# Kernel optimization log

Hardware: AMD Instinct MI355X
Metric: run time of the kernel (lower is better)

The kernel has to match this reference:

```python
import jax, jax.numpy as jnp
import numpy as np

B, F, V_IN = 8, 64, 163842  # icosahedron order 7
V_OUT, K = 40962, 7         # order 6, 1-ring (6 neighbors + self)


def setup_inputs() -> dict:
    key = jax.random.key(0)
    kx, ki = jax.random.split(key)
    x = jax.random.normal(kx, (B, F, V_IN), dtype=jnp.float32)
    neigh_indices = jax.random.randint(ki, (V_OUT, K), 0, V_IN, dtype=jnp.int64)
    return {"x": x, "neigh_indices": neigh_indices}


def reference(x, neigh_indices):
    # Gather fixed-size 1-ring neighborhoods: (B, F, V_OUT, K)
    gathered = x[:, :, neigh_indices]
    # Mean pooling over the neighborhood axis (pooling_type='mean')
    pooled = jnp.mean(gathered, axis=-1)  # (B, F, V_OUT)
    # Original returns (pooled, max_pool_indices=None); indices are None for mean.
    return pooled
```

## Files before the change

### kernel.cpp

```cpp
#include <hip/hip_runtime.h>


typedef float    f4 __attribute__((ext_vector_type(4)));
typedef float    f8 __attribute__((ext_vector_type(8)));
typedef _Float16 h8 __attribute__((ext_vector_type(8)));
typedef unsigned int u4 __attribute__((ext_vector_type(4)));

constexpr int B = 8, F = 64, V_IN = 163842, V_OUT = 40962, K = 7;
constexpr int ROWS = B * F;
constexpr int RG   = 32;
constexpr int NG   = ROWS / RG;
constexpr int TPB  = 256;
constexpr int GPX  = NG / 8;
constexpr int CPB  = 128;
constexpr int IBX  = (V_IN + CPB - 1) / CPB;
constexpr int LSH  = 34;
constexpr int VPB  = 64;
constexpr int VB   = (V_OUT + VPB - 1) / VPB;
constexpr int BLOCKS2 = 8 * GPX * VB;
constexpr size_t XH_BYTES = (size_t)NG * V_IN * 64;

__global__ __launch_bounds__(TPB) void icopool_pack_h(
    const float* __restrict__ x, u4* __restrict__ xH)
{
    __shared__ _Float16 tile[CPB * LSH];
    const int g  = blockIdx.y;
    const int c0 = blockIdx.x * CPB;
    const int t  = threadIdx.x;
    const int r  = t >> 3;
    const int ci = t & 7;

    const float* xr = x + (size_t)(g * RG + r) * V_IN;
    if (c0 + CPB <= V_IN) {
        #pragma unroll
        for (int it = 0; it < 4; ++it) {
            const int c4 = ci * 4 + it * 32;
            const f4 vv = *(const f4*)(xr + c0 + c4);
            tile[(c4 + 0) * LSH + r] = (_Float16)vv.x;
            tile[(c4 + 1) * LSH + r] = (_Float16)vv.y;
            tile[(c4 + 2) * LSH + r] = (_Float16)vv.z;
            tile[(c4 + 3) * LSH + r] = (_Float16)vv.w;
        }
    } else {
        for (int it = 0; it < 4; ++it) {
            const int c4 = ci * 4 + it * 32;
            for (int jj = 0; jj < 4; ++jj) {
                const int c = c0 + c4 + jj;
                tile[(c4 + jj) * LSH + r] =
                    (c < V_IN) ? (_Float16)xr[c] : (_Float16)0.0f;
            }
        }
    }
    __syncthreads();

    const unsigned int* ld = (const unsigned int*)tile;
    u4* dst = xH + ((size_t)g * V_IN + c0) * 4;
    #pragma unroll
    for (int it = 0; it < 2; ++it) {
        const int c   = (t >> 2) + it * 64;
        const int sub = t & 3;
        if (c0 + c < V_IN) {
            u4 w;
            w.x = ld[c * 17 + sub * 4 + 0];
            w.y = ld[c * 17 + sub * 4 + 1];
            w.z = ld[c * 17 + sub * 4 + 2];
            w.w = ld[c * 17 + sub * 4 + 3];
            __builtin_nontemporal_store(w, dst + (size_t)c * 4 + sub);
        }
    }
}

__global__ __launch_bounds__(TPB) void icopool_gather_h(
    const h8* __restrict__ xH,
    const int* __restrict__ nidx,
    float*     __restrict__ out)
{
    const int b   = blockIdx.x;
    const int xcd = b & 7;
    const int j   = b >> 3;
    const int gl  = j / VB;
    const int vb  = j % VB;
    const int sub = threadIdx.x & 3;
    const int lv  = threadIdx.x >> 2;
    const int v   = vb * VPB + lv;
    if (v >= V_OUT) return;
    const int g   = xcd * GPX + gl;

    const int base = v * K;
    const int i0 = nidx[base + 0];
    const int i1 = nidx[base + 1];
    const int i2 = nidx[base + 2];
    const int i3 = nidx[base + 3];
    const int i4 = nidx[base + 4];
    const int i5 = nidx[base + 5];
    const int i6 = nidx[base + 6];

    const h8* s = xH + ((size_t)g * V_IN) * 4 + sub;
    f8 acc = __builtin_convertvector(s[(size_t)i0 * 4], f8);
    acc += __builtin_convertvector(s[(size_t)i1 * 4], f8);
    acc += __builtin_convertvector(s[(size_t)i2 * 4], f8);
    acc += __builtin_convertvector(s[(size_t)i3 * 4], f8);
    acc += __builtin_convertvector(s[(size_t)i4 * 4], f8);
    acc += __builtin_convertvector(s[(size_t)i5 * 4], f8);
    acc += __builtin_convertvector(s[(size_t)i6 * 4], f8);
    acc *= (1.0f / 7.0f);

    float* o = out + (size_t)(g * RG + sub * 8) * V_OUT + v;
    #pragma unroll
    for (int rr = 0; rr < 8; ++rr)
        __builtin_nontemporal_store(acc[rr], o + (size_t)rr * V_OUT);
}

constexpr int RPB  = 2;
constexpr int RGS  = ROWS / RPB;
constexpr int RG_PER_XCD = RGS / 8;
constexpr int VB1  = (V_OUT + TPB - 1) / TPB;
constexpr int BLOCKS_V1  = RGS * VB1;

__global__ __launch_bounds__(TPB) void icopool_gather(
    const float* __restrict__ x,
    const int*   __restrict__ nidx,
    float*       __restrict__ out)
{
    const int b        = blockIdx.x;
    const int xcd      = b & 7;
    const int j        = b >> 3;
    const int rg_local = j / VB1;
    const int vb       = j % VB1;
    const int rg       = xcd * RG_PER_XCD + rg_local;
    const int r0       = rg * RPB;

    const int v = vb * TPB + threadIdx.x;
    if (v >= V_OUT) return;

    const int base = v * K;
    const int i0 = nidx[base + 0];
    const int i1 = nidx[base + 1];
    const int i2 = nidx[base + 2];
    const int i3 = nidx[base + 3];
    const int i4 = nidx[base + 4];
    const int i5 = nidx[base + 5];
    const int i6 = nidx[base + 6];

    #pragma unroll
    for (int r = 0; r < RPB; ++r) {
        const float* xr = x + (size_t)(r0 + r) * V_IN;
        float sum = xr[i0] + xr[i1] + xr[i2] + xr[i3] + xr[i4] + xr[i5] + xr[i6];
        __builtin_nontemporal_store(sum * (1.0f / 7.0f),
                                    out + (size_t)(r0 + r) * V_OUT + v);
    }
}

extern "C" void kernel_launch(void* const* d_in, const int* in_sizes, int n_in,
                              void* d_out, int out_size, void* d_ws, size_t ws_size,
                              hipStream_t stream) {
    const float* x    = (const float*)d_in[0];
    const int*   nidx = (const int*)d_in[1];
    float*       out  = (float*)d_out;

    if (ws_size >= XH_BYTES && d_ws != nullptr) {
        u4* xH = (u4*)d_ws;
        icopool_pack_h<<<dim3(IBX, NG), dim3(TPB), 0, stream>>>(x, xH);
        icopool_gather_h<<<dim3(BLOCKS2), dim3(TPB), 0, stream>>>((const h8*)xH, nidx, out);
    } else {
        icopool_gather<<<dim3(BLOCKS_V1), dim3(TPB), 0, stream>>>(x, nidx, out);
    }
}
```

Before: 578.8 us.

## Repack fp16 input into 16-row groups and gather two groups per thread

The pack kernel now transposes x into fp16 records of 16 rows (32 bytes per vertex) instead of 32 rows (64 bytes), using 256-column tiles and nontemporal loads. The gather kernel assigns each wave 64 consecutive output vertices and has each thread read half of a record from two adjacent groups. The goal is fully coalesced output stores and more loads in flight per thread. The cost is that each random gather access shrinks to 16 bytes, and each record to 32 bytes, which may waste memory-transaction granularity on scattered reads.

```diff
diff --git a/kernel.cpp b/kernel.cpp
--- a/kernel.cpp
+++ b/kernel.cpp
@@ -8,34 +8,34 @@
 
 constexpr int B = 8, F = 64, V_IN = 163842, V_OUT = 40962, K = 7;
 constexpr int ROWS = B * F;
-constexpr int RG   = 32;
+constexpr int RG   = 16;
 constexpr int NG   = ROWS / RG;
 constexpr int TPB  = 256;
 constexpr int GPX  = NG / 8;
-constexpr int CPB  = 128;
+constexpr int CPB  = 256;
 constexpr int IBX  = (V_IN + CPB - 1) / CPB;
-constexpr int LSH  = 34;
-constexpr int VPB  = 64;
+constexpr int LSH  = 18;
+constexpr int VPB  = 128;
 constexpr int VB   = (V_OUT + VPB - 1) / VPB;
-constexpr int BLOCKS2 = 8 * GPX * VB;
-constexpr size_t XH_BYTES = (size_t)NG * V_IN * 64;
-
-__global__ __launch_bounds__(TPB) void icopool_pack_h(
+constexpr int NGL  = 2;
+constexpr int BLOCKS2 = 8 * NGL * VB;
+constexpr size_t XH_BYTES = (size_t)NG * V_IN * 32;
+
+__global__ __launch_bounds__(TPB) void icopool_pack_h16(
     const float* __restrict__ x, u4* __restrict__ xH)
 {
     __shared__ _Float16 tile[CPB * LSH];
     const int g  = blockIdx.y;
     const int c0 = blockIdx.x * CPB;
     const int t  = threadIdx.x;
-    const int r  = t >> 3;
-    const int ci = t & 7;
-
-    const float* xr = x + (size_t)(g * RG + r) * V_IN;
+
     if (c0 + CPB <= V_IN) {
         #pragma unroll
         for (int it = 0; it < 4; ++it) {
-            const int c4 = ci * 4 + it * 32;
-            const f4 vv = *(const f4*)(xr + c0 + c4);
+            const int r  = it * 4 + (t >> 6);
+            const int c4 = (t & 63) * 4;
+            const float* xr = x + (size_t)(g * RG + r) * V_IN + c0;
+            const f4 vv = __builtin_nontemporal_load((const f4*)(xr + c4));
             tile[(c4 + 0) * LSH + r] = (_Float16)vv.x;
             tile[(c4 + 1) * LSH + r] = (_Float16)vv.y;
             tile[(c4 + 2) * LSH + r] = (_Float16)vv.z;
@@ -43,7 +43,9 @@
         }
     } else {
         for (int it = 0; it < 4; ++it) {
-            const int c4 = ci * 4 + it * 32;
+            const int r  = it * 4 + (t >> 6);
+            const int c4 = (t & 63) * 4;
+            const float* xr = x + (size_t)(g * RG + r) * V_IN;
             for (int jj = 0; jj < 4; ++jj) {
                 const int c = c0 + c4 + jj;
                 tile[(c4 + jj) * LSH + r] =
@@ -54,23 +56,24 @@
     __syncthreads();
 
     const unsigned int* ld = (const unsigned int*)tile;
-    u4* dst = xH + ((size_t)g * V_IN + c0) * 4;
+    u4* dst = xH + ((size_t)g * V_IN) * 2;
     #pragma unroll
     for (int it = 0; it < 2; ++it) {
-        const int c   = (t >> 2) + it * 64;
-        const int sub = t & 3;
+        const int c   = (t >> 1) + it * 128;
+        const int sub = t & 1;
         if (c0 + c < V_IN) {
+            const int p = c * 9 + sub * 4;
             u4 w;
-            w.x = ld[c * 17 + sub * 4 + 0];
-            w.y = ld[c * 17 + sub * 4 + 1];
-            w.z = ld[c * 17 + sub * 4 + 2];
-            w.w = ld[c * 17 + sub * 4 + 3];
-            __builtin_nontemporal_store(w, dst + (size_t)c * 4 + sub);
+            w.x = ld[p + 0];
+            w.y = ld[p + 1];
+            w.z = ld[p + 2];
+            w.w = ld[p + 3];
+            dst[((size_t)(c0 + c)) * 2 + sub] = w;
         }
     }
 }
 
-__global__ __launch_bounds__(TPB) void icopool_gather_h(
+__global__ __launch_bounds__(TPB) void icopool_gather_h16(
     const h8* __restrict__ xH,
     const int* __restrict__ nidx,
     float*     __restrict__ out)
@@ -80,11 +83,14 @@
     const int j   = b >> 3;
     const int gl  = j / VB;
     const int vb  = j % VB;
-    const int sub = threadIdx.x & 3;
-    const int lv  = threadIdx.x >> 2;
+    const int t   = threadIdx.x;
+    const int w   = t >> 6;
+    const int sub = w & 1;
+    const int lv  = (t & 63) | ((w >> 1) << 6);
     const int v   = vb * VPB + lv;
     if (v >= V_OUT) return;
-    const int g   = xcd * GPX + gl;
+
+    const int g0  = xcd * GPX + gl * 2;
 
     const int base = v * K;
     const int i0 = nidx[base + 0];
@@ -95,20 +101,48 @@
     const int i5 = nidx[base + 5];
     const int i6 = nidx[base + 6];
 
-    const h8* s = xH + ((size_t)g * V_IN) * 4 + sub;
-    f8 acc = __builtin_convertvector(s[(size_t)i0 * 4], f8);
-    acc += __builtin_convertvector(s[(size_t)i1 * 4], f8);
-    acc += __builtin_convertvector(s[(size_t)i2 * 4], f8);
-    acc += __builtin_convertvector(s[(size_t)i3 * 4], f8);
-    acc += __builtin_convertvector(s[(size_t)i4 * 4], f8);
-    acc += __builtin_convertvector(s[(size_t)i5 * 4], f8);
-    acc += __builtin_convertvector(s[(size_t)i6 * 4], f8);
-    acc *= (1.0f / 7.0f);
-
-    float* o = out + (size_t)(g * RG + sub * 8) * V_OUT + v;
+    const h8* s0 = xH + ((size_t)g0 * V_IN) * 2 + sub;
+    const h8* s1 = s0 + (size_t)V_IN * 2;
+
+    const h8 a0 = s0[(size_t)i0 * 2];
+    const h8 a1 = s0[(size_t)i1 * 2];
+    const h8 a2 = s0[(size_t)i2 * 2];
+    const h8 a3 = s0[(size_t)i3 * 2];
+    const h8 a4 = s0[(size_t)i4 * 2];
+    const h8 a5 = s0[(size_t)i5 * 2];
+    const h8 a6 = s0[(size_t)i6 * 2];
+    const h8 b0 = s1[(size_t)i0 * 2];
+    const h8 b1 = s1[(size_t)i1 * 2];
+    const h8 b2 = s1[(size_t)i2 * 2];
+    const h8 b3 = s1[(size_t)i3 * 2];
+    const h8 b4 = s1[(size_t)i4 * 2];
+    const h8 b5 = s1[(size_t)i5 * 2];
+    const h8 b6 = s1[(size_t)i6 * 2];
+
+    f8 acc0 = __builtin_convertvector(a0, f8);
+    acc0 += __builtin_convertvector(a1, f8);
+    acc0 += __builtin_convertvector(a2, f8);
+    acc0 += __builtin_convertvector(a3, f8);
+    acc0 += __builtin_convertvector(a4, f8);
+    acc0 += __builtin_convertvector(a5, f8);
+    acc0 += __builtin_convertvector(a6, f8);
+    acc0 *= (1.0f / 7.0f);
+    f8 acc1 = __builtin_convertvector(b0, f8);
+    acc1 += __builtin_convertvector(b1, f8);
+    acc1 += __builtin_convertvector(b2, f8);
+    acc1 += __builtin_convertvector(b3, f8);
+    acc1 += __builtin_convertvector(b4, f8);
+    acc1 += __builtin_convertvector(b5, f8);
+    acc1 += __builtin_convertvector(b6, f8);
+    acc1 *= (1.0f / 7.0f);
+
+    float* o0 = out + (size_t)(g0 * RG + sub * 8) * V_OUT + v;
+    float* o1 = o0 + (size_t)RG * V_OUT;
     #pragma unroll
-    for (int rr = 0; rr < 8; ++rr)
-        __builtin_nontemporal_store(acc[rr], o + (size_t)rr * V_OUT);
+    for (int rr = 0; rr < 8; ++rr) {
+        __builtin_nontemporal_store(acc0[rr], o0 + (size_t)rr * V_OUT);
+        __builtin_nontemporal_store(acc1[rr], o1 + (size_t)rr * V_OUT);
+    }
 }
 
 constexpr int RPB  = 2;
@@ -160,8 +194,8 @@
 
     if (ws_size >= XH_BYTES && d_ws != nullptr) {
         u4* xH = (u4*)d_ws;
-        icopool_pack_h<<<dim3(IBX, NG), dim3(TPB), 0, stream>>>(x, xH);
-        icopool_gather_h<<<dim3(BLOCKS2), dim3(TPB), 0, stream>>>((const h8*)xH, nidx, out);
+        icopool_pack_h16<<<dim3(IBX, NG), dim3(TPB), 0, stream>>>(x, xH);
+        icopool_gather_h16<<<dim3(BLOCKS2), dim3(TPB), 0, stream>>>((const h8*)xH, nidx, out);
     } else {
         icopool_gather<<<dim3(BLOCKS_V1), dim3(TPB), 0, stream>>>(x, nidx, out);
     }
```

Result: no change. 582.9 us (+0.7%).
